# Kernel tuning notes

Hardware: AMD Instinct MI355X
Metric: run time of the kernel (lower is better)

## Reference

```python
import jax, jax.numpy as jnp
import numpy as np

NUM_EXPERTS = 64
K = 8
LOAD_BALANCE_SCALE = 0.01
NOISY_STD = 1.0

def setup_inputs() -> dict:
    key = jax.random.key(0)
    k1, k2, k3, k4 = jax.random.split(key, 4)
    N, D, E = 32768, 1024, NUM_EXPERTS
    return {
        "x_flat": jax.random.normal(k1, (N, D), dtype=jnp.float32),
        "gate_w": jax.random.normal(k2, (E, D), dtype=jnp.float32) * (1.0 / np.sqrt(D)),
        "noise_weight": jax.random.normal(k3, (E,), dtype=jnp.float32) * 0.02,
        "noise": jax.random.normal(k4, (N, E), dtype=jnp.float32),
    }

def reference(x_flat, gate_w, noise_weight, noise):
    E = gate_w.shape[0]
    # gate logits: [N, E]
    logits = jnp.einsum('nd,ed->ne', x_flat, gate_w)
    gate_weights = jax.nn.softmax(logits, axis=-1)
    gate_weights_mean = gate_weights.mean(axis=0)  # [E]
    uniform = jnp.full_like(gate_weights_mean, 1.0 / E)
    load_balance_loss = jnp.mean((gate_weights_mean - uniform) ** 2) * LOAD_BALANCE_SCALE
    # noisy logits; noise ~ randn, scaled per-expert by noise_weight
    logits_noisy = logits + (noise * NOISY_STD) * noise_weight
    top_k_vals, top_k_ids = jax.lax.top_k(logits_noisy, K)  # [N, K]
    # scatter top-k logits into -inf canvas, then softmax -> sparse gate weights
    rows = jnp.arange(logits.shape[0])[:, None]
    sparse = jnp.full_like(logits_noisy, -jnp.inf).at[rows, top_k_ids].set(top_k_vals)
    top_k_gated_weights = jax.nn.softmax(sparse, axis=-1)
    return (top_k_gated_weights, top_k_ids, load_balance_loss)
```

## Files before the change

kernel.cpp:

```cpp
#include <hip/hip_runtime.h>
#include <math.h>

#define N_ROWS 32768
#define DIM    1024
#define NE     64
#define KTOP   8


extern "C" __global__ void __launch_bounds__(512, 4)
moe_gate_kernel(const float* __restrict__ x, const float* __restrict__ gw,
                const float* __restrict__ nw, const float* __restrict__ noise,
                float* __restrict__ out0, float* __restrict__ out1,
                float* __restrict__ lossp,
                double* __restrict__ esum, int* __restrict__ ticket) {
    __shared__ __align__(16) float smem[8448];
    __shared__ int isLast;
    float* xt  = smem;
    float* wt  = smem + 4096;
    float* red = smem;
    float* lg  = smem + 4096;

    const int tid  = threadIdx.x;
    const int lane = tid & 63;
    const int wid  = __builtin_amdgcn_readfirstlane(tid >> 6);
    const int er   = lane >> 3;
    const int rr   = lane & 7;
    const int er8  = er * 8;
    const int rr8  = rr * 8;
    const int row0 = blockIdx.x * 64;

    float acc[8][8];
#pragma unroll
    for (int m = 0; m < 8; ++m)
#pragma unroll
        for (int n = 0; n < 8; ++n) acc[m][n] = 0.f;

    const float* gx  = x  + (size_t)(row0 + lane) * DIM + wid * 8;
    const float* gwp = gw + (size_t)lane * DIM + wid * 8;
    float*       xw  = xt + wid * 512 + lane;
    float*       ww  = wt + wid * 512 + lane;
    const float* xr  = xt + wid * 512 + rr8;
    const float* wr  = wt + wid * 512 + er8;

#pragma unroll 1
    for (int rc = 0; rc < 16; ++rc) {
        float px[8], pw[8];
        *(float4*)(px + 0) = *(const float4*)(gx  + rc * 64 + 0);
        *(float4*)(px + 4) = *(const float4*)(gx  + rc * 64 + 4);
        *(float4*)(pw + 0) = *(const float4*)(gwp + rc * 64 + 0);
        *(float4*)(pw + 4) = *(const float4*)(gwp + rc * 64 + 4);
#pragma unroll
        for (int q = 0; q < 8; ++q) {
            xw[q * 64] = px[q];
            ww[q * 64] = pw[q];
        }
#pragma unroll 1
        for (int q = 0; q < 8; ++q) {
            float xf[8], wf[8];
            *(float4*)(xf + 0) = *(const float4*)(xr + q * 64 + 0);
            *(float4*)(xf + 4) = *(const float4*)(xr + q * 64 + 4);
            *(float4*)(wf + 0) = *(const float4*)(wr + q * 64 + 0);
            *(float4*)(wf + 4) = *(const float4*)(wr + q * 64 + 4);
#pragma unroll
            for (int m = 0; m < 8; ++m)
#pragma unroll
                for (int n = 0; n < 8; ++n)
                    acc[m][n] = fmaf(xf[m], wf[n], acc[m][n]);
        }
    }

    __syncthreads();
#pragma unroll
    for (int s = 0; s < 8; ++s) {
        float4 v0 = make_float4(acc[s][0], acc[s][1], acc[s][2], acc[s][3]);
        float4 v1 = make_float4(acc[s][4], acc[s][5], acc[s][6], acc[s][7]);
        *(float4*)(red + wid * 512 + rr * 64 + er8 + 0) = v0;
        *(float4*)(red + wid * 512 + rr * 64 + er8 + 4) = v1;
        __syncthreads();
        {
            const int r2 = tid >> 6, e = tid & 63;
            float t = 0.f;
#pragma unroll
            for (int w = 0; w < 8; ++w) t += red[w * 512 + r2 * 64 + e];
            lg[(r2 * 8 + s) * 65 + e] = t;
        }
        __syncthreads();
    }

    const float nwl = nw[lane];
    float epart = 0.f;

#pragma unroll 1
    for (int i = 0; i < 8; ++i) {
        const int    lrow = wid * 8 + i;
        const size_t grow = (size_t)(row0 + lrow);
        const float  lgv  = lg[lrow * 65 + lane];

        float m = lgv;
#pragma unroll
        for (int off = 32; off; off >>= 1) m = fmaxf(m, __shfl_xor(m, off));
        float p = __expf(lgv - m);
        float s = p;
#pragma unroll
        for (int off = 32; off; off >>= 1) s += __shfl_xor(s, off);
        epart += p / s;

        const float nz    = noise[grow * NE + lane];
        const float noisy = fmaf(nz, nwl, lgv);
        float cur  = noisy;
        bool  sel  = false;
        float mtop = 0.f;
        int   myid = 0;
#pragma unroll
        for (int j = 0; j < KTOP; ++j) {
            float v = cur; int id = lane;
#pragma unroll
            for (int off = 32; off; off >>= 1) {
                float ov = __shfl_xor(v, off);
                int   oi = __shfl_xor(id, off);
                if (ov > v || (ov == v && oi < id)) { v = ov; id = oi; }
            }
            if (j == 0) mtop = v;
            if (lane == id) { sel = true; cur = -INFINITY; }
            if (lane == j) myid = id;
        }

        float swv  = sel ? __expf(noisy - mtop) : 0.f;
        float ssum = swv;
#pragma unroll
        for (int off = 32; off; off >>= 1) ssum += __shfl_xor(ssum, off);

        out0[grow * NE + lane] = swv / ssum;
        if (lane < KTOP) out1[grow * KTOP + lane] = (float)myid;
    }

    __syncthreads();
    red[wid * 64 + lane] = epart;
    __syncthreads();
    if (tid < NE) {
        float t = 0.f;
#pragma unroll
        for (int w = 0; w < 8; ++w) t += red[w * 64 + tid];
        atomicAdd(&esum[tid], (double)t);
        __threadfence();
    }
    __syncthreads();
    if (tid == 0) {
        int t = atomicAdd(ticket, 1);
        isLast = (t == (int)gridDim.x - 1);
        __threadfence();
    }
    __syncthreads();

    if (isLast && tid < NE) {
        double v = atomicAdd(&esum[tid], 0.0);
        double mean = v * (1.0 / 32768.0);
        double d  = mean - (1.0 / 64.0);
        double sq = d * d;
#pragma unroll
        for (int off = 32; off; off >>= 1) sq += __shfl_xor(sq, off);
        if (tid == 0) lossp[0] = (float)(sq * (1.0 / 64.0) * 0.01);
    }
}

extern "C" void kernel_launch(void* const* d_in, const int* in_sizes, int n_in,
                              void* d_out, int out_size, void* d_ws, size_t ws_size,
                              hipStream_t stream) {
    const float* x     = (const float*)d_in[0];
    const float* gw    = (const float*)d_in[1];
    const float* nw    = (const float*)d_in[2];
    const float* noise = (const float*)d_in[3];

    float* out0  = (float*)d_out;
    float* out1  = out0 + (size_t)N_ROWS * NE;
    float* lossp = out1 + (size_t)N_ROWS * KTOP;

    double* esum   = (double*)d_ws;
    int*    ticket = (int*)((char*)d_ws + 512);

    hipMemsetAsync(d_ws, 0, 520, stream);
    moe_gate_kernel<<<N_ROWS / 64, 512, 0, stream>>>(x, gw, nw, noise,
                                                     out0, out1, lossp, esum, ticket);
}
```

Before: 293.7 us.

## Load x rows directly into registers and double-buffer weight fragments from LDS

Each wave now owns a contiguous 128-wide K slice. x fragments are read straight from global memory into registers instead of being staged through LDS, so only gate weights go through shared memory. The inner loop is fully unrolled and ping-pongs between two weight register fragments, overlapping LDS reads with FMAs. This cuts LDS traffic and shared memory size. The cost is less coalesced global x loads, with lanes striding across rows, and higher register pressure.

```diff
diff --git a/kernel.cpp b/kernel.cpp
--- a/kernel.cpp
+++ b/kernel.cpp
@@ -6,6 +6,21 @@
 #define NE     64
 #define KTOP   8
 
+
+#define LOADW(DST, Q) do {                                              \
+    *(float4*)((DST) + 0) = *(const float4*)(ws + (Q) * 64 + er8 + 0);  \
+    *(float4*)((DST) + 4) = *(const float4*)(ws + (Q) * 64 + er8 + 4);  \
+} while (0)
+
+#define FMAQ(W, Q) do {                                                 \
+    _Pragma("unroll")                                                   \
+    for (int m_ = 0; m_ < 8; ++m_) {                                    \
+        const float xv_ = xA[m_ * 4 + ((Q) & 3)];                       \
+        _Pragma("unroll")                                               \
+        for (int n_ = 0; n_ < 8; ++n_)                                  \
+            acc[m_][n_] = fmaf(xv_, (W)[n_], acc[m_][n_]);              \
+    }                                                                   \
+} while (0)
 
 extern "C" __global__ void __launch_bounds__(512, 4)
 moe_gate_kernel(const float* __restrict__ x, const float* __restrict__ gw,
@@ -13,10 +28,9 @@
                 float* __restrict__ out0, float* __restrict__ out1,
                 float* __restrict__ lossp,
                 double* __restrict__ esum, int* __restrict__ ticket) {
-    __shared__ __align__(16) float smem[8448];
+    __shared__ __align__(16) float smem[8256];
     __shared__ int isLast;
-    float* xt  = smem;
-    float* wt  = smem + 4096;
+    float* wt  = smem;
     float* red = smem;
     float* lg  = smem + 4096;
 
@@ -28,6 +42,7 @@
     const int er8  = er * 8;
     const int rr8  = rr * 8;
     const int row0 = blockIdx.x * 64;
+    const int kwb  = wid * 128;
 
     float acc[8][8];
 #pragma unroll
@@ -35,38 +50,41 @@
 #pragma unroll
         for (int n = 0; n < 8; ++n) acc[m][n] = 0.f;
 
-    const float* gx  = x  + (size_t)(row0 + lane) * DIM + wid * 8;
-    const float* gwp = gw + (size_t)lane * DIM + wid * 8;
-    float*       xw  = xt + wid * 512 + lane;
-    float*       ww  = wt + wid * 512 + lane;
-    const float* xr  = xt + wid * 512 + rr8;
-    const float* wr  = wt + wid * 512 + er8;
+    const float* gwp = gw + (size_t)lane * DIM + kwb;
+    float* ws = wt + wid * 512;
+    float* ww = ws + lane;
+    const int voff = (row0 + rr8) * DIM + kwb;
+
+    float xA[32], wf0[8], wf1[8];
 
 #pragma unroll 1
-    for (int rc = 0; rc < 16; ++rc) {
-        float px[8], pw[8];
-        *(float4*)(px + 0) = *(const float4*)(gx  + rc * 64 + 0);
-        *(float4*)(px + 4) = *(const float4*)(gx  + rc * 64 + 4);
-        *(float4*)(pw + 0) = *(const float4*)(gwp + rc * 64 + 0);
-        *(float4*)(pw + 4) = *(const float4*)(gwp + rc * 64 + 4);
-#pragma unroll
-        for (int q = 0; q < 8; ++q) {
-            xw[q * 64] = px[q];
-            ww[q * 64] = pw[q];
-        }
-#pragma unroll 1
-        for (int q = 0; q < 8; ++q) {
-            float xf[8], wf[8];
-            *(float4*)(xf + 0) = *(const float4*)(xr + q * 64 + 0);
-            *(float4*)(xf + 4) = *(const float4*)(xr + q * 64 + 4);
-            *(float4*)(wf + 0) = *(const float4*)(wr + q * 64 + 0);
-            *(float4*)(wf + 4) = *(const float4*)(wr + q * 64 + 4);
-#pragma unroll
-            for (int m = 0; m < 8; ++m)
-#pragma unroll
-                for (int n = 0; n < 8; ++n)
-                    acc[m][n] = fmaf(xf[m], wf[n], acc[m][n]);
-        }
+    for (int rnd = 0; rnd < 16; ++rnd) {
+        const int kof = rnd * 8;
+        float pw[8];
+        *(float4*)(pw + 0) = *(const float4*)(gwp + kof + 0);
+        *(float4*)(pw + 4) = *(const float4*)(gwp + kof + 4);
+#pragma unroll
+        for (int q = 0; q < 8; ++q) ww[q * 64] = pw[q];
+
+#pragma unroll
+        for (int m = 0; m < 8; ++m)
+            *(float4*)(xA + 4 * m) = *(const float4*)(x + m * DIM + voff + kof);
+
+        LOADW(wf0, 0);
+        LOADW(wf1, 1);  FMAQ(wf0, 0);
+        LOADW(wf0, 2);  FMAQ(wf1, 1);
+        LOADW(wf1, 3);  FMAQ(wf0, 2);
+                        FMAQ(wf1, 3);
+
+#pragma unroll
+        for (int m = 0; m < 8; ++m)
+            *(float4*)(xA + 4 * m) = *(const float4*)(x + m * DIM + voff + kof + 4);
+
+        LOADW(wf0, 4);
+        LOADW(wf1, 5);  FMAQ(wf0, 4);
+        LOADW(wf0, 6);  FMAQ(wf1, 5);
+        LOADW(wf1, 7);  FMAQ(wf0, 6);
+                        FMAQ(wf1, 7);
     }
 
     __syncthreads();
```

Measured after the change: 389.8 us. +32.7%, slower.

## Software-pipeline gate GEMM with register prefetch and double-buffered LDS fragments

Applied to the files above, without the earlier changes.

Each wave now owns a contiguous 128-wide slice of the reduction dimension instead of an interleaved one. The next global chunk of x and gate_w is prefetched into registers while the current chunk is staged through LDS. LDS fragment reads are double-buffered so that loads for step q+1 are issued before the FMAs for step q, which is meant to hide global and LDS latency in the dot-product loop. The cross-wave reduction buffer is padded (row stride 68, wave stride 544) to reduce bank conflicts, at the cost of slightly more shared memory and extra registers that could limit occupancy.

```diff
diff --git a/kernel.cpp b/kernel.cpp
--- a/kernel.cpp
+++ b/kernel.cpp
@@ -6,6 +6,22 @@
 #define NE     64
 #define KTOP   8
 
+
+#define LOADQ(XB, WB, Q) do {                                        \
+    *(float4*)((XB) + 0) = *(const float4*)(rd_x + (Q) * 64 + 0);    \
+    *(float4*)((XB) + 4) = *(const float4*)(rd_x + (Q) * 64 + 4);    \
+    *(float4*)((WB) + 0) = *(const float4*)(rd_w + (Q) * 64 + 0);    \
+    *(float4*)((WB) + 4) = *(const float4*)(rd_w + (Q) * 64 + 4);    \
+} while (0)
+
+#define FMAQ(XB, WB) do {                                            \
+    _Pragma("unroll")                                                \
+    for (int m_ = 0; m_ < 8; ++m_) {                                 \
+        _Pragma("unroll")                                            \
+        for (int n_ = 0; n_ < 8; ++n_)                               \
+            acc[m_][n_] = fmaf((XB)[m_], (WB)[n_], acc[m_][n_]);     \
+    }                                                                \
+} while (0)
 
 extern "C" __global__ void __launch_bounds__(512, 4)
 moe_gate_kernel(const float* __restrict__ x, const float* __restrict__ gw,
@@ -13,12 +29,12 @@
                 float* __restrict__ out0, float* __restrict__ out1,
                 float* __restrict__ lossp,
                 double* __restrict__ esum, int* __restrict__ ticket) {
-    __shared__ __align__(16) float smem[8448];
+    __shared__ __align__(16) float smem[8512];
     __shared__ int isLast;
     float* xt  = smem;
     float* wt  = smem + 4096;
     float* red = smem;
-    float* lg  = smem + 4096;
+    float* lg  = smem + 4352;
 
     const int tid  = threadIdx.x;
     const int lane = tid & 63;
@@ -28,6 +44,7 @@
     const int er8  = er * 8;
     const int rr8  = rr * 8;
     const int row0 = blockIdx.x * 64;
+    const int kwb  = wid * 128;
 
     float acc[8][8];
 #pragma unroll
@@ -35,38 +52,41 @@
 #pragma unroll
         for (int n = 0; n < 8; ++n) acc[m][n] = 0.f;
 
-    const float* gx  = x  + (size_t)(row0 + lane) * DIM + wid * 8;
-    const float* gwp = gw + (size_t)lane * DIM + wid * 8;
-    float*       xw  = xt + wid * 512 + lane;
-    float*       ww  = wt + wid * 512 + lane;
-    const float* xr  = xt + wid * 512 + rr8;
-    const float* wr  = wt + wid * 512 + er8;
+    const float* gx   = x  + (size_t)(row0 + lane) * DIM + kwb;
+    const float* gwp  = gw + (size_t)lane * DIM + kwb;
+    float*       ws_x = xt + wid * 512 + lane;
+    float*       ws_w = wt + wid * 512 + lane;
+    const float* rd_x = xt + wid * 512 + rr8;
+    const float* rd_w = wt + wid * 512 + er8;
+
+    float px[8], pw[8], xf0[8], xf1[8], wf0[8], wf1[8];
+    *(float4*)(px + 0) = *(const float4*)(gx + 0);
+    *(float4*)(px + 4) = *(const float4*)(gx + 4);
+    *(float4*)(pw + 0) = *(const float4*)(gwp + 0);
+    *(float4*)(pw + 4) = *(const float4*)(gwp + 4);
 
 #pragma unroll 1
-    for (int rc = 0; rc < 16; ++rc) {
-        float px[8], pw[8];
-        *(float4*)(px + 0) = *(const float4*)(gx  + rc * 64 + 0);
-        *(float4*)(px + 4) = *(const float4*)(gx  + rc * 64 + 4);
-        *(float4*)(pw + 0) = *(const float4*)(gwp + rc * 64 + 0);
-        *(float4*)(pw + 4) = *(const float4*)(gwp + rc * 64 + 4);
+    for (int rnd = 0; rnd < 16; ++rnd) {
 #pragma unroll
         for (int q = 0; q < 8; ++q) {
-            xw[q * 64] = px[q];
-            ww[q * 64] = pw[q];
-        }
-#pragma unroll 1
-        for (int q = 0; q < 8; ++q) {
-            float xf[8], wf[8];
-            *(float4*)(xf + 0) = *(const float4*)(xr + q * 64 + 0);
-            *(float4*)(xf + 4) = *(const float4*)(xr + q * 64 + 4);
-            *(float4*)(wf + 0) = *(const float4*)(wr + q * 64 + 0);
-            *(float4*)(wf + 4) = *(const float4*)(wr + q * 64 + 4);
-#pragma unroll
-            for (int m = 0; m < 8; ++m)
-#pragma unroll
-                for (int n = 0; n < 8; ++n)
-                    acc[m][n] = fmaf(xf[m], wf[n], acc[m][n]);
-        }
+            ws_x[q * 64] = px[q];
+            ws_w[q * 64] = pw[q];
+        }
+        if (rnd < 15) {
+            *(float4*)(px + 0) = *(const float4*)(gx + (rnd + 1) * 8 + 0);
+            *(float4*)(px + 4) = *(const float4*)(gx + (rnd + 1) * 8 + 4);
+            *(float4*)(pw + 0) = *(const float4*)(gwp + (rnd + 1) * 8 + 0);
+            *(float4*)(pw + 4) = *(const float4*)(gwp + (rnd + 1) * 8 + 4);
+        }
+        LOADQ(xf0, wf0, 0);
+        LOADQ(xf1, wf1, 1);  FMAQ(xf0, wf0);
+        LOADQ(xf0, wf0, 2);  FMAQ(xf1, wf1);
+        LOADQ(xf1, wf1, 3);  FMAQ(xf0, wf0);
+        LOADQ(xf0, wf0, 4);  FMAQ(xf1, wf1);
+        LOADQ(xf1, wf1, 5);  FMAQ(xf0, wf0);
+        LOADQ(xf0, wf0, 6);  FMAQ(xf1, wf1);
+        LOADQ(xf1, wf1, 7);  FMAQ(xf0, wf0);
+                             FMAQ(xf1, wf1);
     }
 
     __syncthreads();
@@ -74,14 +94,14 @@
     for (int s = 0; s < 8; ++s) {
         float4 v0 = make_float4(acc[s][0], acc[s][1], acc[s][2], acc[s][3]);
         float4 v1 = make_float4(acc[s][4], acc[s][5], acc[s][6], acc[s][7]);
-        *(float4*)(red + wid * 512 + rr * 64 + er8 + 0) = v0;
-        *(float4*)(red + wid * 512 + rr * 64 + er8 + 4) = v1;
+        *(float4*)(red + wid * 544 + rr * 68 + er8 + 0) = v0;
+        *(float4*)(red + wid * 544 + rr * 68 + er8 + 4) = v1;
         __syncthreads();
         {
             const int r2 = tid >> 6, e = tid & 63;
             float t = 0.f;
 #pragma unroll
-            for (int w = 0; w < 8; ++w) t += red[w * 512 + r2 * 64 + e];
+            for (int w = 0; w < 8; ++w) t += red[w * 544 + r2 * 68 + e];
             lg[(r2 * 8 + s) * 65 + e] = t;
         }
         __syncthreads();
```

Result: slower. 335.2 us (+14.1%).
